# Performance work log

Measured on AMD Instinct MI355X. Metric: run time of the kernel, lower is better.

## Reference

```python
import jax, jax.numpy as jnp
from jax import lax
import numpy as np

NB = 4      # num_blocks
C = 1024    # model_channels
H = 16      # num_heads
P = 2       # patch_size
OUT_C = 64  # FinalLayer out_channels


def _sincos_1d(d, pos):
    omega = np.arange(d // 2, dtype=np.float64) / (d / 2.0)
    omega = 1.0 / 10000 ** omega
    out = np.einsum('m,d->md', pos.reshape(-1), omega)
    return np.concatenate([np.sin(out), np.cos(out)], axis=1)


def _sincos_2d(embed_dim, h, w):
    gh = np.arange(h, dtype=np.float32)
    gw = np.arange(w, dtype=np.float32)
    grid = np.stack(np.meshgrid(gw, gh), axis=0).reshape(2, 1, h, w)
    emb = np.concatenate([_sincos_1d(embed_dim // 2, grid[0]),
                          _sincos_1d(embed_dim // 2, grid[1])], axis=1)
    return jnp.asarray(emb, dtype=jnp.float32)  # (h*w, embed_dim)


def _ln(x, g, b, eps):
    mu = jnp.mean(x, axis=-1, keepdims=True)
    var = jnp.mean(jnp.square(x - mu), axis=-1, keepdims=True)
    y = (x - mu) * lax.rsqrt(var + eps)
    if g is not None:
        y = y * g + b
    return y


def _conv3x3(x, w, b):
    y = lax.conv_general_dilated(x, w, (1, 1), [(1, 1), (1, 1)],
                                 dimension_numbers=('NCHW', 'OIHW', 'NCHW'))
    return y + b[None, :, None, None]


def _forward(x, qkv_w, qkv_b, proj_w, proj_b, nq_g, nq_b, nk_g, nk_b,
             n1_g, n1_b, n2_g, n2_b, fc1_w, fc1_b, fc2_w, fc2_b,
             fin_w, fin_b, c1_w, c1_b, c2_w, c2_b):
    bs, l, c = x.shape
    h = w = int(np.sqrt(l))
    d = c // H
    scale = 1.0 / np.sqrt(d)
    x = x + _sincos_2d(c, h, w)[None]  # add 2D sincos pos embed
    for i in range(NB):
        # --- QK-norm attention ---
        res = x
        hn = _ln(x, n1_g[i], n1_b[i], 1e-5)
        qkv = hn @ qkv_w[i] + qkv_b[i]                 # (bs, l, 3c)
        q, k, v = jnp.split(qkv, 3, axis=-1)
        to_heads = lambda t: t.reshape(bs, l, H, d).transpose(0, 2, 1, 3)  # bhnd
        q = _ln(to_heads(q), nq_g[i], nq_b[i], 1e-5)
        k = _ln(to_heads(k), nk_g[i], nk_b[i], 1e-5)
        v = to_heads(v)
        attn = jax.nn.softmax(jnp.einsum('bhnd,bhmd->bhnm', q, k) * scale, axis=-1)
        o = jnp.einsum('bhnm,bhmd->bhnd', attn, v)
        o = o.transpose(0, 2, 1, 3).reshape(bs, l, c)
        x = res + (o @ proj_w[i] + proj_b[i])
        # --- MLP ---
        hn2 = _ln(x, n2_g[i], n2_b[i], 1e-5)
        mlp = jax.nn.gelu(hn2 @ fc1_w[i] + fc1_b[i], approximate=False) @ fc2_w[i] + fc2_b[i]
        x = x + mlp
    # --- final layer ---
    xf = _ln(x, None, None, 1e-6)
    xf = xf @ fin_w + fin_b                            # (bs, l, P*P*OUT_C)
    # --- unpatchify: last dim is flattened (c, p, p) ---
    xf = xf.reshape(bs, h, w, OUT_C, P, P)
    xf = jnp.einsum('bhwcpq->bhpwqc', xf).reshape(bs, h * P, w * P, OUT_C)
    xf = xf.transpose(0, 3, 1, 2)                      # (bs, 64, 64, 64)
    y = jax.nn.relu(_conv3x3(xf, c1_w, c1_b))
    y = _conv3x3(y, c2_w, c2_b)
    return y


def setup_inputs() -> dict:
    key = jax.random.key(0)
    ks = jax.random.split(key, 12)
    s = 0.02
    f = jnp.float32
    inp = {
        'x': jax.random.normal(ks[0], (2, 1024, C), f),
        'qkv_w': s * jax.random.normal(ks[1], (NB, C, 3 * C), f),
        'qkv_b': jnp.zeros((NB, 3 * C), f),
        'proj_w': s * jax.random.normal(ks[2], (NB, C, C), f),
        'proj_b': jnp.zeros((NB, C), f),
        'nq_g': jnp.ones((NB, C // H), f),
        'nq_b': jnp.zeros((NB, C // H), f),
        'nk_g': jnp.ones((NB, C // H), f),
        'nk_b': jnp.zeros((NB, C // H), f),
        'n1_g': jnp.ones((NB, C), f),
        'n1_b': jnp.zeros((NB, C), f),
        'n2_g': jnp.ones((NB, C), f),
        'n2_b': jnp.zeros((NB, C), f),
        'fc1_w': s * jax.random.normal(ks[3], (NB, C, 4 * C), f),
        'fc1_b': jnp.zeros((NB, 4 * C), f),
        'fc2_w': s * jax.random.normal(ks[4], (NB, 4 * C, C), f),
        'fc2_b': jnp.zeros((NB, C), f),
        'fin_w': s * jax.random.normal(ks[5], (C, P * P * OUT_C), f),
        'fin_b': jnp.zeros((P * P * OUT_C,), f),
        'c1_w': s * jax.random.normal(ks[6], (16, OUT_C, 3, 3), f),
        'c1_b': jnp.zeros((16,), f),
        'c2_w': s * jax.random.normal(ks[7], (3, 16, 3, 3), f),
        'c2_b': jnp.zeros((3,), f),
    }
    return inp


def reference(x, qkv_w, qkv_b, proj_w, proj_b, nq_g, nq_b, nk_g, nk_b,
              n1_g, n1_b, n2_g, n2_b, fc1_w, fc1_b, fc2_w, fc2_b,
              fin_w, fin_b, c1_w, c1_b, c2_w, c2_b):
    return _forward(x, qkv_w, qkv_b, proj_w, proj_b, nq_g, nq_b, nk_g, nk_b,
                    n1_g, n1_b, n2_g, n2_b, fc1_w, fc1_b, fc2_w, fc2_b,
                    fin_w, fin_b, c1_w, c1_b, c2_w, c2_b)
```

## Files before the change

### kernel.cpp

```cpp
#include <hip/hip_runtime.h>
#include <hip/hip_bf16.h>
#include <math.h>

typedef float floatx4 __attribute__((ext_vector_type(4)));
typedef short bf16x8 __attribute__((ext_vector_type(8)));

__device__ __forceinline__ unsigned short f2bf(float x) {
    union { float f; unsigned int u; } v; v.f = x;
    unsigned int r = v.u + 0x7fffu + ((v.u >> 16) & 1u);
    return (unsigned short)(r >> 16);
}

__device__ __forceinline__ void load_lds16(const void* g, void* l) {
    __builtin_amdgcn_global_load_lds(
        (const __attribute__((address_space(1))) unsigned int*)(uintptr_t)g,
        (__attribute__((address_space(3))) unsigned int*)(uintptr_t)l, 16, 0, 0);
}

__global__ void posembed_kernel(const float* __restrict__ xin, float* __restrict__ xb) {
    int idx = blockIdx.x * 256 + threadIdx.x;
    int c = idx & 1023;
    int n = (idx >> 10) & 1023;
    int pos = (c < 512) ? (n & 31) : (n >> 5);
    int cc = c & 511;
    int k = cc & 255;
    double om = exp(-(double)k * (9.210340371976184 / 256.0));
    double arg = (double)pos * om;
    float e = (float)((cc < 256) ? sin(arg) : cos(arg));
    xb[idx] = xin[idx] + e;
}

__global__ __launch_bounds__(256) void ln_kernel(const float* __restrict__ X,
                                                 unsigned short* __restrict__ Y,
                                                 const float* __restrict__ g,
                                                 const float* __restrict__ b,
                                                 float eps, int affine) {
    int row = blockIdx.x;
    const float4* xr = (const float4*)(X + (size_t)row * 1024);
    float4 x = xr[threadIdx.x];
    float s = x.x + x.y + x.z + x.w;
    float sq = x.x * x.x + x.y * x.y + x.z * x.z + x.w * x.w;
    __shared__ float red[8];
    #pragma unroll
    for (int off = 32; off; off >>= 1) { s += __shfl_xor(s, off); sq += __shfl_xor(sq, off); }
    int wid = threadIdx.x >> 6, lane = threadIdx.x & 63;
    if (!lane) { red[wid] = s; red[wid + 4] = sq; }
    __syncthreads();
    s = red[0] + red[1] + red[2] + red[3];
    sq = red[4] + red[5] + red[6] + red[7];
    float mu = s * (1.f / 1024.f);
    float var = sq * (1.f / 1024.f) - mu * mu;
    float rs = rsqrtf(var + eps);
    int c = threadIdx.x * 4;
    float4 y;
    if (affine) {
        y.x = (x.x - mu) * rs * g[c + 0] + b[c + 0];
        y.y = (x.y - mu) * rs * g[c + 1] + b[c + 1];
        y.z = (x.z - mu) * rs * g[c + 2] + b[c + 2];
        y.w = (x.w - mu) * rs * g[c + 3] + b[c + 3];
    } else {
        y.x = (x.x - mu) * rs; y.y = (x.y - mu) * rs;
        y.z = (x.z - mu) * rs; y.w = (x.w - mu) * rs;
    }
    ushort4 o;
    o.x = f2bf(y.x); o.y = f2bf(y.y); o.z = f2bf(y.z); o.w = f2bf(y.w);
    *(ushort4*)(Y + (size_t)row * 1024 + c) = o;
}

__global__ __launch_bounds__(256) void qkvprep_kernel(const float* __restrict__ qkv,
                                                      const float* __restrict__ nqg,
                                                      const float* __restrict__ nqb,
                                                      const float* __restrict__ nkg,
                                                      const float* __restrict__ nkb,
                                                      unsigned short* __restrict__ Qb,
                                                      unsigned short* __restrict__ Kb,
                                                      unsigned short* __restrict__ Vt) {
    __shared__ float t[64][65];
    int tid = threadIdx.x;
    int l0 = blockIdx.x * 64, h = blockIdx.y, b = blockIdx.z;
    for (int i = tid; i < 4096; i += 256) {
        int lr = i >> 6, dd = i & 63;
        t[lr][dd] = qkv[((size_t)(b * 1024 + l0 + lr)) * 3072 + 2048 + h * 64 + dd];
    }
    __syncthreads();
    for (int i = tid; i < 4096; i += 256) {
        int dd = i >> 6, lc = i & 63;
        Vt[((size_t)((b * 16 + h) * 64 + dd)) * 1024 + l0 + lc] = f2bf(t[lc][dd]);
    }
    int wave = tid >> 6, lane = tid & 63;
    float gq = nqg[lane], bq = nqb[lane], gk = nkg[lane], bk = nkb[lane];
    for (int i = 0; i < 16; i++) {
        int l = l0 + wave + 4 * i;
        const float* base = qkv + (size_t)(b * 1024 + l) * 3072 + h * 64 + lane;
        #pragma unroll
        for (int part = 0; part < 2; part++) {
            float v = base[part * 1024];
            float s = v, sq = v * v;
            #pragma unroll
            for (int off = 32; off; off >>= 1) { s += __shfl_xor(s, off); sq += __shfl_xor(sq, off); }
            float mu = s * (1.f / 64.f);
            float var = sq * (1.f / 64.f) - mu * mu;
            float rs = rsqrtf(var + 1e-5f);
            float y = (v - mu) * rs * (part ? gk : gq) + (part ? bk : bq);
            unsigned short* dst = part ? Kb : Qb;
            dst[(size_t)(b * 1024 + l) * 1024 + h * 64 + lane] = f2bf(y * (part ? 1.f : 0.125f));
        }
    }
}

__global__ __launch_bounds__(256) void attn_mfma(const unsigned short* __restrict__ Qb,
                                                 const unsigned short* __restrict__ Kb,
                                                 const unsigned short* __restrict__ Vt,
                                                 unsigned short* __restrict__ ob) {
    __shared__ short Ks[64 * 64];
    __shared__ short Vs[64 * 64];
    __shared__ short Pl[4][16 * 72];
    int tid = threadIdx.x;
    int lane = tid & 63, wave = tid >> 6;
    int ln16 = lane & 15, q = lane >> 4;
    int b = blockIdx.z, h = blockIdx.y, q0 = blockIdx.x * 64;

    const unsigned short* qrow = Qb + ((size_t)(b * 1024 + q0 + wave * 16 + ln16)) * 1024 + h * 64;
    bf16x8 qf0 = *(const bf16x8*)(qrow + q * 8);
    bf16x8 qf1 = *(const bf16x8*)(qrow + 32 + q * 8);

    floatx4 o[4];
    #pragma unroll
    for (int td = 0; td < 4; td++) o[td] = (floatx4){0.f, 0.f, 0.f, 0.f};
    float mrow[4] = {-1e30f, -1e30f, -1e30f, -1e30f};
    float lrow[4] = {0.f, 0.f, 0.f, 0.f};

    const unsigned short* kbase0 = Kb + ((size_t)(b * 1024)) * 1024 + h * 64;
    const unsigned short* vbase0 = Vt + ((size_t)((b * 16 + h) * 64)) * 1024;

    for (int ch = 0; ch < 16; ch++) {
        int l0 = ch * 64;
        __syncthreads();
        #pragma unroll
        for (int it = 0; it < 2; it++) {
            int j = tid + it * 256;
            int row = j >> 3, g = j & 7;
            load_lds16(kbase0 + (size_t)(l0 + row) * 1024 + g * 8, &Ks[j * 8]);
            load_lds16(vbase0 + (size_t)row * 1024 + l0 + g * 8, &Vs[j * 8]);
        }
        __syncthreads();

        floatx4 s[4];
        #pragma unroll
        for (int t = 0; t < 4; t++) {
            s[t] = (floatx4){0.f, 0.f, 0.f, 0.f};
            bf16x8 kf0 = *(const bf16x8*)&Ks[(t * 16 + ln16) * 64 + q * 8];
            bf16x8 kf1 = *(const bf16x8*)&Ks[(t * 16 + ln16) * 64 + 32 + q * 8];
            s[t] = __builtin_amdgcn_mfma_f32_16x16x32_bf16(qf0, kf0, s[t], 0, 0, 0);
            s[t] = __builtin_amdgcn_mfma_f32_16x16x32_bf16(qf1, kf1, s[t], 0, 0, 0);
        }
        float cm[4], rs[4], p[4][4];
        #pragma unroll
        for (int r = 0; r < 4; r++)
            cm[r] = fmaxf(fmaxf(s[0][r], s[1][r]), fmaxf(s[2][r], s[3][r]));
        #pragma unroll
        for (int off = 1; off < 16; off <<= 1) {
            #pragma unroll
            for (int r = 0; r < 4; r++) cm[r] = fmaxf(cm[r], __shfl_xor(cm[r], off));
        }
        #pragma unroll
        for (int r = 0; r < 4; r++) {
            float mnew = fmaxf(mrow[r], cm[r]);
            float alpha = __expf(mrow[r] - mnew);
            mrow[r] = mnew;
            rs[r] = 0.f;
            #pragma unroll
            for (int t = 0; t < 4; t++) {
                p[t][r] = __expf(s[t][r] - mnew);
                rs[r] += p[t][r];
            }
            lrow[r] *= alpha;
            #pragma unroll
            for (int td = 0; td < 4; td++) o[td][r] *= alpha;
        }
        #pragma unroll
        for (int off = 1; off < 16; off <<= 1) {
            #pragma unroll
            for (int r = 0; r < 4; r++) rs[r] += __shfl_xor(rs[r], off);
        }
        #pragma unroll
        for (int r = 0; r < 4; r++) lrow[r] += rs[r];

        short* pw = &Pl[wave][0];
        #pragma unroll
        for (int t = 0; t < 4; t++)
            #pragma unroll
            for (int r = 0; r < 4; r++)
                pw[(q * 4 + r) * 72 + t * 16 + ln16] = (short)f2bf(p[t][r]);
        __syncthreads();
        bf16x8 pf0 = *(const bf16x8*)&pw[ln16 * 72 + q * 8];
        bf16x8 pf1 = *(const bf16x8*)&pw[ln16 * 72 + 32 + q * 8];
        #pragma unroll
        for (int td = 0; td < 4; td++) {
            bf16x8 vf0 = *(const bf16x8*)&Vs[(td * 16 + ln16) * 64 + q * 8];
            bf16x8 vf1 = *(const bf16x8*)&Vs[(td * 16 + ln16) * 64 + 32 + q * 8];
            o[td] = __builtin_amdgcn_mfma_f32_16x16x32_bf16(pf0, vf0, o[td], 0, 0, 0);
            o[td] = __builtin_amdgcn_mfma_f32_16x16x32_bf16(pf1, vf1, o[td], 0, 0, 0);
        }
    }
    #pragma unroll
    for (int td = 0; td < 4; td++) {
        #pragma unroll
        for (int r = 0; r < 4; r++) {
            int row = q0 + wave * 16 + q * 4 + r;
            int col = h * 64 + td * 16 + ln16;
            ob[((size_t)(b * 1024 + row)) * 1024 + col] = f2bf(o[td][r] / lrow[r]);
        }
    }
}

__global__ __launch_bounds__(256) void wtrans_kernel(const float* __restrict__ in,
                                                     unsigned short* __restrict__ out,
                                                     int K, int N) {
    __shared__ float t[64][65];
    int n0 = blockIdx.x * 64, k0 = blockIdx.y * 64, z = blockIdx.z;
    in  += (size_t)z * K * N;
    out += (size_t)z * N * K;
    for (int i = threadIdx.x; i < 4096; i += 256) {
        int kr = i >> 6, nc = i & 63;
        t[kr][nc] = in[(size_t)(k0 + kr) * N + n0 + nc];
    }
    __syncthreads();
    for (int i = threadIdx.x; i < 4096; i += 256) {
        int nr = i >> 6, kc = i & 63;
        out[(size_t)(n0 + nr) * K + k0 + kc] = f2bf(t[kc][nr]);
    }
}

template <int BM, int BN, int WM, int WN, int ACT, bool ADDC, bool OUTBF16, bool SPLITK>
__global__ __launch_bounds__(256) void gemm_bf16(const unsigned short* __restrict__ A,
                                                 const unsigned short* __restrict__ Bt,
                                                 const float* __restrict__ bias,
                                                 float* __restrict__ Cf,
                                                 unsigned short* __restrict__ Cb,
                                                 int M, int N, int K, int lda) {
    constexpr int MT = BM / (WM * 16);
    constexpr int NT = BN / (WN * 16);
    __shared__ short As[BM * 64];
    __shared__ short Bs[BN * 64];
    int tid = threadIdx.x;
    int lane = tid & 63, wave = tid >> 6;
    int wm = wave / WN, wn = wave % WN;
    int ln16 = lane & 15, q = lane >> 4;
    int m0 = blockIdx.y * BM, n0 = blockIdx.x * BN;
    int kOff = SPLITK ? blockIdx.z * K : 0;

    floatx4 acc[MT][NT];
    #pragma unroll
    for (int i = 0; i < MT; i++)
        #pragma unroll
        for (int j = 0; j < NT; j++) acc[i][j] = (floatx4){0.f, 0.f, 0.f, 0.f};

    int kSteps = K >> 6;
    for (int ks = 0; ks < kSteps; ks++) {
        int k0 = kOff + (ks << 6);
        #pragma unroll
        for (int it = 0; it < BM / 32; it++) {
            int i = tid + it * 256;
            int row = i >> 3, gc = (i & 7) ^ (row & 7);
            load_lds16(A + (size_t)(m0 + row) * lda + k0 + gc * 8, &As[i * 8]);
        }
        #pragma unroll
        for (int it = 0; it < BN / 32; it++) {
            int i = tid + it * 256;
            int row = i >> 3, gc = (i & 7) ^ (row & 7);
            load_lds16(Bt + (size_t)(n0 + row) * lda + k0 + gc * 8, &Bs[i * 8]);
        }
        __syncthreads();
        bf16x8 af[2][MT], bf[2][NT];
        #pragma unroll
        for (int h = 0; h < 2; h++) {
            #pragma unroll
            for (int mi = 0; mi < MT; mi++) {
                int row = wm * (BM / WM) + mi * 16 + ln16;
                af[h][mi] = *(const bf16x8*)&As[row * 64 + (((h * 4 + q) ^ (row & 7)) * 8)];
            }
            #pragma unroll
            for (int ni = 0; ni < NT; ni++) {
                int row = wn * (BN / WN) + ni * 16 + ln16;
                bf[h][ni] = *(const bf16x8*)&Bs[row * 64 + (((h * 4 + q) ^ (row & 7)) * 8)];
            }
        }
        #pragma unroll
        for (int h = 0; h < 2; h++)
            #pragma unroll
            for (int mi = 0; mi < MT; mi++)
                #pragma unroll
                for (int ni = 0; ni < NT; ni++)
                    acc[mi][ni] = __builtin_amdgcn_mfma_f32_16x16x32_bf16(af[h][mi], bf[h][ni], acc[mi][ni], 0, 0, 0);
        __syncthreads();
    }

    int q4 = q * 4;
    float* Cp = SPLITK ? (Cf + (size_t)blockIdx.z * M * N) : Cf;
    #pragma unroll
    for (int ni = 0; ni < NT; ni++) {
        int col = n0 + wn * (BN / WN) + ni * 16 + ln16;
        float bv = SPLITK ? 0.f : bias[col];
        #pragma unroll
        for (int mi = 0; mi < MT; mi++) {
            #pragma unroll
            for (int r = 0; r < 4; r++) {
                int row = m0 + wm * (BM / WM) + mi * 16 + q4 + r;
                size_t off = (size_t)row * N + col;
                float v = acc[mi][ni][r] + bv;
                if (!SPLITK && ACT == 1) v = 0.5f * v * (1.f + erff(v * 0.70710678118654752f));
                if (!SPLITK && ADDC) v += Cf[off];
                if (!SPLITK && OUTBF16) Cb[off] = f2bf(v);
                else Cp[off] = v;
            }
        }
    }
}

__global__ __launch_bounds__(256) void skreduce_kernel(const float* __restrict__ P,
                                                       const float* __restrict__ bias,
                                                       float* __restrict__ xb) {
    int idx = blockIdx.x * 256 + threadIdx.x;
    float4 a = ((const float4*)P)[idx];
    float4 b = ((const float4*)P)[idx + 524288];
    float4 x = ((float4*)xb)[idx];
    const float4 bb = *(const float4*)(bias + (idx & 255) * 4);
    x.x += a.x + b.x + bb.x;
    x.y += a.y + b.y + bb.y;
    x.z += a.z + b.z + bb.z;
    x.w += a.w + b.w + bb.w;
    ((float4*)xb)[idx] = x;
}

__global__ void unpatchify_kernel(const float* __restrict__ xf, float* __restrict__ img) {
    int idx = blockIdx.x * 256 + threadIdx.x;
    int x = idx & 63, y = (idx >> 6) & 63, ch = (idx >> 12) & 63, b = idx >> 18;
    int hh = y >> 1, ww = x >> 1, p = y & 1, qq = x & 1;
    img[idx] = xf[((size_t)b * 1024 + hh * 32 + ww) * 256 + ch * 4 + p * 2 + qq];
}

__global__ __launch_bounds__(256) void conv1_kernel(const float* __restrict__ img,
                                                    const float* __restrict__ w,
                                                    const float* __restrict__ bias,
                                                    float* __restrict__ out) {
    __shared__ float Ls[64 * 3 * 66];
    __shared__ float Ws[16 * 580];
    int tid = threadIdx.x;
    int y = blockIdx.x, b = blockIdx.y;
    for (int i = tid; i < 9216; i += 256) {
        int oc = i / 576, rem = i % 576;
        Ws[oc * 580 + rem] = w[i];
    }
    for (int i = tid; i < 12288; i += 256) {
        int r = i >> 6, x = i & 63;
        int ic = r / 3, ky = r % 3;
        int yy = y + ky - 1;
        float v = (yy >= 0 && yy < 64) ? img[((size_t)(b * 64 + ic) * 64 + yy) * 64 + x] : 0.f;
        Ls[(ic * 3 + ky) * 66 + x + 1] = v;
        if (x == 0)  Ls[(ic * 3 + ky) * 66 + 0]  = 0.f;
        if (x == 63) Ls[(ic * 3 + ky) * 66 + 65] = 0.f;
    }
    __syncthreads();
    int oc = tid >> 4, xg = (tid & 15) * 4;
    float bv = bias[oc];
    float acc0 = bv, acc1 = bv, acc2 = bv, acc3 = bv;
    for (int ic = 0; ic < 64; ic++) {
        const float* wr = &Ws[oc * 580 + ic * 9];
        float w00 = wr[0], w01 = wr[1], w02 = wr[2];
        float w10 = wr[3], w11 = wr[4], w12 = wr[5];
        float w20 = wr[6], w21 = wr[7], w22 = wr[8];
        const float* l0 = &Ls[(ic * 3 + 0) * 66 + xg];
        const float* l1 = &Ls[(ic * 3 + 1) * 66 + xg];
        const float* l2 = &Ls[(ic * 3 + 2) * 66 + xg];
        float a0 = l0[0], a1 = l0[1], a2 = l0[2], a3 = l0[3], a4 = l0[4], a5 = l0[5];
        float b0 = l1[0], b1 = l1[1], b2 = l1[2], b3 = l1[3], b4 = l1[4], b5 = l1[5];
        float c0 = l2[0], c1 = l2[1], c2 = l2[2], c3 = l2[3], c4 = l2[4], c5 = l2[5];
        acc0 += a0*w00 + a1*w01 + a2*w02 + b0*w10 + b1*w11 + b2*w12 + c0*w20 + c1*w21 + c2*w22;
        acc1 += a1*w00 + a2*w01 + a3*w02 + b1*w10 + b2*w11 + b3*w12 + c1*w20 + c2*w21 + c3*w22;
        acc2 += a2*w00 + a3*w01 + a4*w02 + b2*w10 + b3*w11 + b4*w12 + c2*w20 + c3*w21 + c4*w22;
        acc3 += a3*w00 + a4*w01 + a5*w02 + b3*w10 + b4*w11 + b5*w12 + c3*w20 + c4*w21 + c5*w22;
    }
    float* op = out + (((size_t)(b * 16 + oc) * 64 + y) * 64 + xg);
    op[0] = fmaxf(acc0, 0.f);
    op[1] = fmaxf(acc1, 0.f);
    op[2] = fmaxf(acc2, 0.f);
    op[3] = fmaxf(acc3, 0.f);
}

__global__ __launch_bounds__(256) void conv2_kernel(const float* __restrict__ in,
                                                    const float* __restrict__ w,
                                                    const float* __restrict__ bias,
                                                    float* __restrict__ out) {
    __shared__ float Ls[16 * 3 * 66];
    __shared__ float Ws[3 * 160];
    int tid = threadIdx.x;
    int y = blockIdx.x, b = blockIdx.y;
    for (int i = tid; i < 432; i += 256) {
        int oc = i / 144, rem = i % 144;
        Ws[oc * 160 + rem] = w[i];
    }
    for (int i = tid; i < 3072; i += 256) {
        int r = i >> 6, x = i & 63;
        int ic = r / 3, ky = r % 3;
        int yy = y + ky - 1;
        float v = (yy >= 0 && yy < 64) ? in[((size_t)(b * 16 + ic) * 64 + yy) * 64 + x] : 0.f;
        Ls[(ic * 3 + ky) * 66 + x + 1] = v;
        if (x == 0)  Ls[(ic * 3 + ky) * 66 + 0]  = 0.f;
        if (x == 63) Ls[(ic * 3 + ky) * 66 + 65] = 0.f;
    }
    __syncthreads();
    int oc = tid >> 6, x = tid & 63;
    if (oc < 3) {
        float acc = bias[oc];
        for (int ic = 0; ic < 16; ic++) {
            const float* wr = &Ws[oc * 160 + ic * 9];
            const float* l0 = &Ls[(ic * 3 + 0) * 66 + x];
            const float* l1 = &Ls[(ic * 3 + 1) * 66 + x];
            const float* l2 = &Ls[(ic * 3 + 2) * 66 + x];
            acc += l0[0]*wr[0] + l0[1]*wr[1] + l0[2]*wr[2]
                 + l1[0]*wr[3] + l1[1]*wr[4] + l1[2]*wr[5]
                 + l2[0]*wr[6] + l2[1]*wr[7] + l2[2]*wr[8];
        }
        out[((size_t)(b * 3 + oc) * 64 + y) * 64 + x] = acc;
    }
}

extern "C" void kernel_launch(void* const* d_in, const int* in_sizes, int n_in,
                              void* d_out, int out_size, void* d_ws, size_t ws_size,
                              hipStream_t stream) {
    const float* x_in   = (const float*)d_in[0];
    const float* qkv_w  = (const float*)d_in[1];
    const float* qkv_b  = (const float*)d_in[2];
    const float* proj_w = (const float*)d_in[3];
    const float* proj_b = (const float*)d_in[4];
    const float* nq_g   = (const float*)d_in[5];
    const float* nq_b   = (const float*)d_in[6];
    const float* nk_g   = (const float*)d_in[7];
    const float* nk_b   = (const float*)d_in[8];
    const float* n1_g   = (const float*)d_in[9];
    const float* n1_b   = (const float*)d_in[10];
    const float* n2_g   = (const float*)d_in[11];
    const float* n2_b   = (const float*)d_in[12];
    const float* fc1_w  = (const float*)d_in[13];
    const float* fc1_b  = (const float*)d_in[14];
    const float* fc2_w  = (const float*)d_in[15];
    const float* fc2_b  = (const float*)d_in[16];
    const float* fin_w  = (const float*)d_in[17];
    const float* fin_b  = (const float*)d_in[18];
    const float* c1_w   = (const float*)d_in[19];
    const float* c1_b   = (const float*)d_in[20];
    const float* c2_w   = (const float*)d_in[21];
    const float* c2_b   = (const float*)d_in[22];
    float* out = (float*)d_out;

    char* w = (char*)d_ws;
    float* xb           = (float*)w;          w += (size_t)2 * 1024 * 1024 * 4;
    unsigned short* hnb = (unsigned short*)w; w += (size_t)2 * 1024 * 1024 * 2;
    float* qkv          = (float*)w;          w += (size_t)2 * 1024 * 3072 * 4;
    unsigned short* obb = (unsigned short*)w; w += (size_t)2 * 1024 * 1024 * 2;
    unsigned short* mhb = (unsigned short*)w; w += (size_t)2 * 1024 * 4096 * 2;
    float* xf           = (float*)w;          w += (size_t)2 * 1024 * 256 * 4;
    float* img          = (float*)w;          w += (size_t)2 * 64 * 64 * 64 * 4;
    float* c1o          = (float*)w;          w += (size_t)2 * 16 * 64 * 64 * 4;
    unsigned short* Qb  = (unsigned short*)w; w += (size_t)2 * 1024 * 1024 * 2;
    unsigned short* Kb  = (unsigned short*)w; w += (size_t)2 * 1024 * 1024 * 2;
    unsigned short* Vt  = (unsigned short*)w; w += (size_t)2 * 16 * 64 * 1024 * 2;
    float* skb          = (float*)w;          w += (size_t)2 * 2048 * 1024 * 4;
    unsigned short* WQ  = (unsigned short*)w; w += (size_t)4 * 1024 * 3072 * 2;
    unsigned short* WP  = (unsigned short*)w; w += (size_t)4 * 1024 * 1024 * 2;
    unsigned short* W1  = (unsigned short*)w; w += (size_t)4 * 1024 * 4096 * 2;
    unsigned short* W2  = (unsigned short*)w; w += (size_t)4 * 4096 * 1024 * 2;
    unsigned short* WF  = (unsigned short*)w; w += (size_t)1024 * 256 * 2;

    wtrans_kernel<<<dim3(48, 16, 4), 256, 0, stream>>>(qkv_w, WQ, 1024, 3072);
    wtrans_kernel<<<dim3(16, 16, 4), 256, 0, stream>>>(proj_w, WP, 1024, 1024);
    wtrans_kernel<<<dim3(64, 16, 4), 256, 0, stream>>>(fc1_w, W1, 1024, 4096);
    wtrans_kernel<<<dim3(16, 64, 4), 256, 0, stream>>>(fc2_w, W2, 4096, 1024);
    wtrans_kernel<<<dim3(4, 16, 1), 256, 0, stream>>>(fin_w, WF, 1024, 256);

    posembed_kernel<<<8192, 256, 0, stream>>>(x_in, xb);

    for (int i = 0; i < 4; i++) {
        ln_kernel<<<2048, 256, 0, stream>>>(xb, hnb, n1_g + i * 1024, n1_b + i * 1024, 1e-5f, 1);
        gemm_bf16<64, 128, 2, 2, 0, false, false, false><<<dim3(24, 32), 256, 0, stream>>>(
            hnb, WQ + (size_t)i * 3072 * 1024, qkv_b + i * 3072, qkv, nullptr, 2048, 3072, 1024, 1024);
        qkvprep_kernel<<<dim3(16, 16, 2), 256, 0, stream>>>(
            qkv, nq_g + i * 64, nq_b + i * 64, nk_g + i * 64, nk_b + i * 64, Qb, Kb, Vt);
        attn_mfma<<<dim3(16, 16, 2), 256, 0, stream>>>(Qb, Kb, Vt, obb);
        gemm_bf16<64, 64, 2, 2, 0, true, false, false><<<dim3(16, 32), 256, 0, stream>>>(
            obb, WP + (size_t)i * 1024 * 1024, proj_b + i * 1024, xb, nullptr, 2048, 1024, 1024, 1024);
        ln_kernel<<<2048, 256, 0, stream>>>(xb, hnb, n2_g + i * 1024, n2_b + i * 1024, 1e-5f, 1);
        gemm_bf16<64, 128, 2, 2, 1, false, true, false><<<dim3(32, 32), 256, 0, stream>>>(
            hnb, W1 + (size_t)i * 4096 * 1024, fc1_b + i * 4096, nullptr, mhb, 2048, 4096, 1024, 1024);
        gemm_bf16<64, 64, 2, 2, 0, false, false, true><<<dim3(16, 32, 2), 256, 0, stream>>>(
            mhb, W2 + (size_t)i * 1024 * 4096, fc2_b + i * 1024, skb, nullptr, 2048, 1024, 2048, 4096);
        skreduce_kernel<<<2048, 256, 0, stream>>>(skb, fc2_b + i * 1024, xb);
    }

    ln_kernel<<<2048, 256, 0, stream>>>(xb, hnb, nullptr, nullptr, 1e-6f, 0);
    gemm_bf16<64, 64, 2, 2, 0, false, false, false><<<dim3(4, 32), 256, 0, stream>>>(
        hnb, WF, fin_b, xf, nullptr, 2048, 256, 1024, 1024);
    unpatchify_kernel<<<2048, 256, 0, stream>>>(xf, img);
    conv1_kernel<<<dim3(64, 2), 256, 0, stream>>>(img, c1_w, c1_b, c1o);
    conv2_kernel<<<dim3(64, 2), 256, 0, stream>>>(c1o, c2_w, c2_b, out);
}
```

Measured before the change: 1.065 ms.

## Load attention K/V fragments directly from global, enlarge GEMM tiles, float posembed

The attention kernel stops staging K and V tiles in shared memory and instead loads each wave's MFMA fragments straight from global memory into registers. This removes two block-wide barriers per chunk plus the barrier before the P·V step. Several GEMM launches move to larger 128x128 or 64x128 tiles with smaller grids, trading occupancy for more data reuse per tile. The positional-embedding kernel switches from double to float transcendentals, which slightly changes numerics. With K/V read per wave, the four waves in a block each fetch the same data, which raises global/L2 traffic, and the larger tiles leave fewer blocks to fill the CUs.

```diff
diff --git a/kernel.cpp b/kernel.cpp
--- a/kernel.cpp
+++ b/kernel.cpp
@@ -24,9 +24,9 @@
     int pos = (c < 512) ? (n & 31) : (n >> 5);
     int cc = c & 511;
     int k = cc & 255;
-    double om = exp(-(double)k * (9.210340371976184 / 256.0));
-    double arg = (double)pos * om;
-    float e = (float)((cc < 256) ? sin(arg) : cos(arg));
+    float om = expf(-(float)k * (9.210340371976184f / 256.0f));
+    float arg = (float)pos * om;
+    float e = (cc < 256) ? sinf(arg) : cosf(arg);
     xb[idx] = xin[idx] + e;
 }
 
@@ -112,8 +112,6 @@
                                                  const unsigned short* __restrict__ Kb,
                                                  const unsigned short* __restrict__ Vt,
                                                  unsigned short* __restrict__ ob) {
-    __shared__ short Ks[64 * 64];
-    __shared__ short Vs[64 * 64];
     __shared__ short Pl[4][16 * 72];
     int tid = threadIdx.x;
     int lane = tid & 63, wave = tid >> 6;
@@ -130,29 +128,31 @@
     float mrow[4] = {-1e30f, -1e30f, -1e30f, -1e30f};
     float lrow[4] = {0.f, 0.f, 0.f, 0.f};
 
-    const unsigned short* kbase0 = Kb + ((size_t)(b * 1024)) * 1024 + h * 64;
-    const unsigned short* vbase0 = Vt + ((size_t)((b * 16 + h) * 64)) * 1024;
+    const unsigned short* kbase = Kb + ((size_t)(b * 1024 + ln16)) * 1024 + h * 64 + q * 8;
+    const unsigned short* vbase = Vt + ((size_t)((b * 16 + h) * 64 + ln16)) * 1024 + q * 8;
 
     for (int ch = 0; ch < 16; ch++) {
         int l0 = ch * 64;
-        __syncthreads();
-        #pragma unroll
-        for (int it = 0; it < 2; it++) {
-            int j = tid + it * 256;
-            int row = j >> 3, g = j & 7;
-            load_lds16(kbase0 + (size_t)(l0 + row) * 1024 + g * 8, &Ks[j * 8]);
-            load_lds16(vbase0 + (size_t)row * 1024 + l0 + g * 8, &Vs[j * 8]);
-        }
-        __syncthreads();
-
+        bf16x8 kf[4][2];
+        #pragma unroll
+        for (int t = 0; t < 4; t++) {
+            const unsigned short* kp = kbase + (size_t)(l0 + t * 16) * 1024;
+            kf[t][0] = *(const bf16x8*)kp;
+            kf[t][1] = *(const bf16x8*)(kp + 32);
+        }
         floatx4 s[4];
         #pragma unroll
         for (int t = 0; t < 4; t++) {
             s[t] = (floatx4){0.f, 0.f, 0.f, 0.f};
-            bf16x8 kf0 = *(const bf16x8*)&Ks[(t * 16 + ln16) * 64 + q * 8];
-            bf16x8 kf1 = *(const bf16x8*)&Ks[(t * 16 + ln16) * 64 + 32 + q * 8];
-            s[t] = __builtin_amdgcn_mfma_f32_16x16x32_bf16(qf0, kf0, s[t], 0, 0, 0);
-            s[t] = __builtin_amdgcn_mfma_f32_16x16x32_bf16(qf1, kf1, s[t], 0, 0, 0);
+            s[t] = __builtin_amdgcn_mfma_f32_16x16x32_bf16(qf0, kf[t][0], s[t], 0, 0, 0);
+            s[t] = __builtin_amdgcn_mfma_f32_16x16x32_bf16(qf1, kf[t][1], s[t], 0, 0, 0);
+        }
+        bf16x8 vf[4][2];
+        #pragma unroll
+        for (int td = 0; td < 4; td++) {
+            const unsigned short* vp = vbase + (size_t)(td * 16) * 1024 + l0;
+            vf[td][0] = *(const bf16x8*)vp;
+            vf[td][1] = *(const bf16x8*)(vp + 32);
         }
         float cm[4], rs[4], p[4][4];
         #pragma unroll
@@ -192,15 +192,12 @@
             #pragma unroll
             for (int r = 0; r < 4; r++)
                 pw[(q * 4 + r) * 72 + t * 16 + ln16] = (short)f2bf(p[t][r]);
-        __syncthreads();
         bf16x8 pf0 = *(const bf16x8*)&pw[ln16 * 72 + q * 8];
         bf16x8 pf1 = *(const bf16x8*)&pw[ln16 * 72 + 32 + q * 8];
         #pragma unroll
         for (int td = 0; td < 4; td++) {
-            bf16x8 vf0 = *(const bf16x8*)&Vs[(td * 16 + ln16) * 64 + q * 8];
-            bf16x8 vf1 = *(const bf16x8*)&Vs[(td * 16 + ln16) * 64 + 32 + q * 8];
-            o[td] = __builtin_amdgcn_mfma_f32_16x16x32_bf16(pf0, vf0, o[td], 0, 0, 0);
-            o[td] = __builtin_amdgcn_mfma_f32_16x16x32_bf16(pf1, vf1, o[td], 0, 0, 0);
+            o[td] = __builtin_amdgcn_mfma_f32_16x16x32_bf16(pf0, vf[td][0], o[td], 0, 0, 0);
+            o[td] = __builtin_amdgcn_mfma_f32_16x16x32_bf16(pf1, vf[td][1], o[td], 0, 0, 0);
         }
     }
     #pragma unroll
@@ -483,17 +480,17 @@
 
     for (int i = 0; i < 4; i++) {
         ln_kernel<<<2048, 256, 0, stream>>>(xb, hnb, n1_g + i * 1024, n1_b + i * 1024, 1e-5f, 1);
-        gemm_bf16<64, 128, 2, 2, 0, false, false, false><<<dim3(24, 32), 256, 0, stream>>>(
+        gemm_bf16<128, 128, 2, 2, 0, false, false, false><<<dim3(24, 16), 256, 0, stream>>>(
             hnb, WQ + (size_t)i * 3072 * 1024, qkv_b + i * 3072, qkv, nullptr, 2048, 3072, 1024, 1024);
         qkvprep_kernel<<<dim3(16, 16, 2), 256, 0, stream>>>(
             qkv, nq_g + i * 64, nq_b + i * 64, nk_g + i * 64, nk_b + i * 64, Qb, Kb, Vt);
         attn_mfma<<<dim3(16, 16, 2), 256, 0, stream>>>(Qb, Kb, Vt, obb);
-        gemm_bf16<64, 64, 2, 2, 0, true, false, false><<<dim3(16, 32), 256, 0, stream>>>(
+        gemm_bf16<64, 128, 2, 2, 0, true, false, false><<<dim3(8, 32), 256, 0, stream>>>(
             obb, WP + (size_t)i * 1024 * 1024, proj_b + i * 1024, xb, nullptr, 2048, 1024, 1024, 1024);
         ln_kernel<<<2048, 256, 0, stream>>>(xb, hnb, n2_g + i * 1024, n2_b + i * 1024, 1e-5f, 1);
-        gemm_bf16<64, 128, 2, 2, 1, false, true, false><<<dim3(32, 32), 256, 0, stream>>>(
+        gemm_bf16<128, 128, 2, 2, 1, false, true, false><<<dim3(32, 16), 256, 0, stream>>>(
             hnb, W1 + (size_t)i * 4096 * 1024, fc1_b + i * 4096, nullptr, mhb, 2048, 4096, 1024, 1024);
-        gemm_bf16<64, 64, 2, 2, 0, false, false, true><<<dim3(16, 32, 2), 256, 0, stream>>>(
+        gemm_bf16<128, 128, 2, 2, 0, false, false, true><<<dim3(8, 16, 2), 256, 0, stream>>>(
             mhb, W2 + (size_t)i * 1024 * 4096, fc2_b + i * 1024, skb, nullptr, 2048, 1024, 2048, 4096);
         skreduce_kernel<<<2048, 256, 0, stream>>>(skb, fc2_b + i * 1024, xb);
     }
```

Measured after the change: 1.220 ms. 1.15x slower.
